# Optimization experiments

Measured on AMD Instinct MI355X. Metric: run time of the kernel, lower is better.

## Reference

```python
import jax, jax.numpy as jnp
import numpy as np

CHUNK = 64  # chunk_size from init


def _fused_chunk_fwd(q, k, v, scale, chunk):
    # q,k,v: [B,S,H,D]
    B, S, H, D = q.shape
    NT = S // chunk
    # -> [NT, B, H, chunk, D] for scan over chunks
    def to_chunks(x):
        return x.reshape(B, NT, chunk, H, D).transpose(1, 0, 3, 2, 4)
    qc, kc, vc = to_chunks(q), to_chunks(k), to_chunks(v)
    mask = jnp.tril(jnp.ones((chunk, chunk), dtype=q.dtype))  # row >= col (inclusive)

    def step(h, xs):
        qi, ki, vi = xs  # each [B,H,chunk,D]
        qs = qi * scale
        # intra-chunk causal attention scores (no softmax: linear attention)
        s = jnp.einsum('bhqd,bhkd->bhqk', qs, ki) * mask
        # intra-chunk contribution + inter-chunk recurrent state contribution
        o = jnp.einsum('bhqk,bhke->bhqe', s, vi) + jnp.einsum('bhqd,bhde->bhqe', qs, h)
        # state update: h += K^T V  (strictly after producing this chunk's output)
        h = h + jnp.einsum('bhcd,bhce->bhde', ki, vi)
        return h, o

    h0 = jnp.zeros((B, H, D, D), dtype=jnp.float32)
    hf, oc = jax.lax.scan(step, h0, (qc, kc, vc))
    # oc: [NT,B,H,chunk,D] -> [B,S,H,D]
    o = oc.transpose(1, 0, 3, 2, 4).reshape(B, S, H, D)
    return o, hf


def setup_inputs() -> dict:
    key = jax.random.key(0)
    kq, kk, kv = jax.random.split(key, 3)
    B, S, H, D = 2, 4096, 16, 128
    q = jax.random.normal(kq, (B, S, H, D), dtype=jnp.float32)
    k = jax.random.normal(kk, (B, S, H, D), dtype=jnp.float32)
    v = jax.random.normal(kv, (B, S, H, D), dtype=jnp.float32)
    return {"q": q, "k": k, "v": v}


def reference(q, k, v):
    D = q.shape[-1]
    scale = D ** (-0.5)
    o, final_state = _fused_chunk_fwd(q, k, v, scale, CHUNK)
    return o, final_state
```

## Files before the change

### kernel.cpp

```cpp
#include <hip/hip_runtime.h>
#include <math.h>

#define BB 2
#define SS 4096
#define HH 16
#define DD 128
#define CK 64
#define NTC 64
#define HD 2048
#define SQ 136
#define ST 72

typedef __attribute__((ext_vector_type(8))) short bh8;
typedef __attribute__((ext_vector_type(16))) float fx16;

#define MFMA32(a, b, c) __builtin_amdgcn_mfma_f32_32x32x16_bf16(a, b, c, 0, 0, 0)

__device__ inline unsigned short f2bf(float f) {
    unsigned int u = __float_as_uint(f);
    return (unsigned short)((u + 0x7FFFu + ((u >> 16) & 1u)) >> 16);
}
__device__ inline unsigned int pk2(float a, float b) {
    return (unsigned int)f2bf(a) | ((unsigned int)f2bf(b) << 16);
}

#define SWAP32(x, y) asm("v_permlane32_swap_b32 %0, %1" : "+v"(x), "+v"(y))

#define MKFRAG(dst, cc, O) { \
    unsigned a0_ = pk2(cc[(O)+0], cc[(O)+1]), a1_ = pk2(cc[(O)+2], cc[(O)+3]); \
    unsigned a2_ = pk2(cc[(O)+4], cc[(O)+5]), a3_ = pk2(cc[(O)+6], cc[(O)+7]); \
    SWAP32(a0_, a2_); SWAP32(a1_, a3_); \
    union { unsigned u[4]; bh8 v; } r_; \
    r_.u[0] = a0_; r_.u[1] = a1_; r_.u[2] = a2_; r_.u[3] = a3_; \
    dst = r_.v; }

__global__ __launch_bounds__(512, 4) void ksum_kernel(const float* __restrict__ k,
                                                      const float* __restrict__ v,
                                                      float* __restrict__ G,
                                                      int CPG, int NG) {
    int g = blockIdx.x, h = blockIdx.y, b = blockIdx.z;
    int t = threadIdx.x, l = t & 63, w = t >> 6, hi = l >> 5, lm = l & 31;
    int dbp = 2 * (w >> 2), eb = w & 3;
    __shared__ short lkT[2][128 * ST];
    __shared__ short lvT[2][128 * ST];
    fx16 h0 = {}, h1 = {};
    long hbase = ((long)b * SS) * HD + (long)h * DD;
    float kt[16], vt[16];

#define KLOAD(cc) { long base_ = hbase + (long)(g * CPG + (cc)) * CK * HD; \
    _Pragma("unroll") for (int i = 0; i < 8; ++i) { int it = t + 512 * i; \
        int e = (it & 31) + 32 * (it >> 10); int c2 = (it >> 5) & 31; \
        long ga = base_ + (long)(2 * c2) * HD + e; \
        kt[2*i] = k[ga]; kt[2*i+1] = k[ga + HD]; \
        vt[2*i] = v[ga]; vt[2*i+1] = v[ga + HD]; } }

#define KSTAGE(pn) { \
    _Pragma("unroll") for (int i = 0; i < 8; ++i) { int it = t + 512 * i; \
        int e = (it & 31) + 32 * (it >> 10); int c2 = (it >> 5) & 31; \
        *(unsigned*)&lkT[pn][e * ST + 2 * c2] = pk2(kt[2*i], kt[2*i+1]); \
        *(unsigned*)&lvT[pn][e * ST + 2 * c2] = pk2(vt[2*i], vt[2*i+1]); } }

    KLOAD(0); KSTAGE(0); if (CPG > 1) KLOAD(1);
    __syncthreads();
    int p = 0;
    for (int c = 0; c < CPG; ++c) {
        if (c + 1 < CPG) KSTAGE(p ^ 1);
        if (c + 2 < CPG) KLOAD(c + 2);
        bh8 Bv0 = *(const bh8*)&lvT[p][(32*eb+lm)*ST +  0 + 8*hi];
        bh8 Bv1 = *(const bh8*)&lvT[p][(32*eb+lm)*ST + 16 + 8*hi];
        bh8 Bv2 = *(const bh8*)&lvT[p][(32*eb+lm)*ST + 32 + 8*hi];
        bh8 Bv3 = *(const bh8*)&lvT[p][(32*eb+lm)*ST + 48 + 8*hi];
#define KM4(hx, db) { \
        bh8 A0_ = *(const bh8*)&lkT[p][(32*(db)+lm)*ST +  0 + 8*hi]; hx = MFMA32(A0_, Bv0, hx); \
        bh8 A1_ = *(const bh8*)&lkT[p][(32*(db)+lm)*ST + 16 + 8*hi]; hx = MFMA32(A1_, Bv1, hx); \
        bh8 A2_ = *(const bh8*)&lkT[p][(32*(db)+lm)*ST + 32 + 8*hi]; hx = MFMA32(A2_, Bv2, hx); \
        bh8 A3_ = *(const bh8*)&lkT[p][(32*(db)+lm)*ST + 48 + 8*hi]; hx = MFMA32(A3_, Bv3, hx); }
        KM4(h0, dbp) KM4(h1, dbp + 1)
        __syncthreads();
        p ^= 1;
    }
    float* Gp = G + ((long)(b * HH + h) * NG + g) * (DD * DD);
    long t0 = (long)((dbp) * 4 + eb) * 1024 + l * 16;
    long t1 = (long)((dbp + 1) * 4 + eb) * 1024 + l * 16;
#pragma unroll
    for (int q4 = 0; q4 < 4; ++q4) {
        *(float4*)&Gp[t0 + 4*q4] = make_float4(h0[4*q4], h0[4*q4+1], h0[4*q4+2], h0[4*q4+3]);
        *(float4*)&Gp[t1 + 4*q4] = make_float4(h1[4*q4], h1[4*q4+1], h1[4*q4+2], h1[4*q4+3]);
    }
}

__global__ __launch_bounds__(256) void prefix_kernel(float* __restrict__ G,
                                                     float* __restrict__ hf,
                                                     int NG) {
    int tid = blockIdx.x * 256 + threadIdx.x;
    int bh = tid >> 11;
    int fl = (tid & 2047) * 8;
    float* Gb = G + (long)bh * NG * (DD * DD) + fl;
    float4 a0 = make_float4(0.f, 0.f, 0.f, 0.f), a1 = a0;
    for (int g = 0; g < NG; ++g) {
        float* p = Gb + (long)g * (DD * DD);
        float4 v0 = *(float4*)p;
        float4 v1 = *(float4*)(p + 4);
        *(float4*)p       = a0;
        *(float4*)(p + 4) = a1;
        a0.x += v0.x; a0.y += v0.y; a0.z += v0.z; a0.w += v0.w;
        a1.x += v1.x; a1.y += v1.y; a1.z += v1.z; a1.w += v1.w;
    }
    float acc[8] = {a0.x, a0.y, a0.z, a0.w, a1.x, a1.y, a1.z, a1.w};
    float* hb = hf + (long)bh * (DD * DD);
    int tile = fl >> 10, li = (fl >> 4) & 63;
#pragma unroll
    for (int j = 0; j < 8; ++j) {
        int rg = (fl & 15) + j;
        int d = 32 * (tile >> 2) + (rg & 3) + 8 * (rg >> 2) + 4 * (li >> 5);
        int e = 32 * (tile & 3) + (li & 31);
        hb[d * DD + e] = acc[j];
    }
}

__global__ __launch_bounds__(512, 2) void scan_kernel(const float* __restrict__ q,
                                                      const float* __restrict__ kk,
                                                      const float* __restrict__ vv,
                                                      const float* __restrict__ G,
                                                      float* __restrict__ o,
                                                      int CPG, int NG, float scale) {
    int g = blockIdx.x, h = blockIdx.y, b = blockIdx.z;
    int t = threadIdx.x, l = t & 63, w = t >> 6, hi = l >> 5, lm = l & 31;
    int rb = w >> 2, eb = w & 3;
    __shared__ short lq [2][64 * SQ];
    __shared__ short lk [2][64 * SQ];
    __shared__ short lkT[2][128 * ST];
    __shared__ short lvT[2][128 * ST];

    fx16 h0 = {}, h1 = {}, h2 = {}, h3 = {};
    {
        const float* Gp = G + ((long)(b * HH + h) * NG + g) * (DD * DD);
#define GINIT(hx, db) { const float* p_ = Gp + (long)((db) * 4 + eb) * 1024 + l * 16; \
        _Pragma("unroll") for (int q4 = 0; q4 < 4; ++q4) { \
            float4 x_ = *(const float4*)&p_[4*q4]; \
            hx[4*q4] = x_.x; hx[4*q4+1] = x_.y; hx[4*q4+2] = x_.z; hx[4*q4+3] = x_.w; } }
        GINIT(h0, 0) GINIT(h1, 1) GINIT(h2, 2) GINIT(h3, 3)
    }

    long hbase = ((long)b * SS) * HD + (long)h * DD;
    float4 qv[4], kv[4];
    float kt[16], vt[16];
    int r8 = t >> 3, c8 = t & 7;

#define SLOAD(cc) { long base_ = hbase + (long)(g * CPG + (cc)) * CK * HD; \
    _Pragma("unroll") for (int j = 0; j < 4; ++j) { \
        long ga = base_ + (long)r8 * HD + 4 * c8 + 32 * j; \
        qv[j] = *(const float4*)&q[ga]; kv[j] = *(const float4*)&kk[ga]; } \
    _Pragma("unroll") for (int i = 0; i < 8; ++i) { int it = t + 512 * i; \
        int e = (it & 31) + 32 * (it >> 10); int c2 = (it >> 5) & 31; \
        long ga = base_ + (long)(2 * c2) * HD + e; \
        kt[2*i] = kk[ga]; kt[2*i+1] = kk[ga + HD]; \
        vt[2*i] = vv[ga]; vt[2*i+1] = vv[ga + HD]; } }

#define SSTAGE(pn) { \
    _Pragma("unroll") for (int j = 0; j < 4; ++j) { \
        uint2 uq_; uq_.x = pk2(qv[j].x * scale, qv[j].y * scale); \
        uq_.y = pk2(qv[j].z * scale, qv[j].w * scale); \
        *(uint2*)&lq[pn][r8 * SQ + 4 * c8 + 32 * j] = uq_; \
        uint2 uk_; uk_.x = pk2(kv[j].x, kv[j].y); uk_.y = pk2(kv[j].z, kv[j].w); \
        *(uint2*)&lk[pn][r8 * SQ + 4 * c8 + 32 * j] = uk_; } \
    _Pragma("unroll") for (int i = 0; i < 8; ++i) { int it = t + 512 * i; \
        int e = (it & 31) + 32 * (it >> 10); int c2 = (it >> 5) & 31; \
        *(unsigned*)&lkT[pn][e * ST + 2 * c2] = pk2(kt[2*i], kt[2*i+1]); \
        *(unsigned*)&lvT[pn][e * ST + 2 * c2] = pk2(vt[2*i], vt[2*i+1]); } }

    SLOAD(0); SSTAGE(0); if (CPG > 1) SLOAD(1);
    __syncthreads();
    int p = 0;

    for (int c = 0; c < CPG; ++c) {
        long base = hbase + (long)(g * CPG + c) * CK * HD;
        if (c + 1 < CPG) SSTAGE(p ^ 1);

        fx16 sa0 = {}, sa1 = {};
#pragma unroll
        for (int ks = 0; ks < 8; ++ks) {
            bh8 Bq = *(const bh8*)&lq[p][(32*rb+lm)*SQ + 16*ks + 8*hi];
            bh8 A0 = *(const bh8*)&lk[p][lm*SQ + 16*ks + 8*hi];
            sa0 = MFMA32(A0, Bq, sa0);
            if (rb) {
                bh8 A1 = *(const bh8*)&lk[p][(32+lm)*SQ + 16*ks + 8*hi];
                sa1 = MFMA32(A1, Bq, sa1);
            }
        }
        bh8 fS0, fS1, fS2, fS3;
        {
            float ms[16];
            int rr = 32 * rb + lm;
            if (rb == 0) {
#pragma unroll
                for (int rg = 0; rg < 16; ++rg) {
                    int cc_ = (rg & 3) + 8 * (rg >> 2) + 4 * hi;
                    ms[rg] = (cc_ <= rr) ? sa0[rg] : 0.f;
                }
                MKFRAG(fS0, ms, 0) MKFRAG(fS1, ms, 8)
                fS2 = fS0; fS3 = fS1;
            } else {
                MKFRAG(fS0, sa0, 0) MKFRAG(fS1, sa0, 8)
#pragma unroll
                for (int rg = 0; rg < 16; ++rg) {
                    int cc_ = 32 + (rg & 3) + 8 * (rg >> 2) + 4 * hi;
                    ms[rg] = (cc_ <= rr) ? sa1[rg] : 0.f;
                }
                MKFRAG(fS2, ms, 0) MKFRAG(fS3, ms, 8)
            }
        }
        if (c + 2 < CPG) SLOAD(c + 2);

        bh8 Bv0 = *(const bh8*)&lvT[p][(32*eb+lm)*ST +  0 + 8*hi];
        bh8 Bv1 = *(const bh8*)&lvT[p][(32*eb+lm)*ST + 16 + 8*hi];
        bh8 Bv2 = *(const bh8*)&lvT[p][(32*eb+lm)*ST + 32 + 8*hi];
        bh8 Bv3 = *(const bh8*)&lvT[p][(32*eb+lm)*ST + 48 + 8*hi];

        fx16 oa = {};
        oa = MFMA32(fS0, Bv0, oa);
        oa = MFMA32(fS1, Bv1, oa);
        if (rb) {
            oa = MFMA32(fS2, Bv2, oa);
            oa = MFMA32(fS3, Bv3, oa);
        }
#define M3STEP(hx, db) { \
        bh8 Aq0 = *(const bh8*)&lq[p][(32*rb+lm)*SQ + 16*(2*(db)) + 8*hi]; \
        bh8 Bh0; MKFRAG(Bh0, hx, 0); oa = MFMA32(Aq0, Bh0, oa); \
        bh8 Aq1 = *(const bh8*)&lq[p][(32*rb+lm)*SQ + 16*(2*(db)+1) + 8*hi]; \
        bh8 Bh1; MKFRAG(Bh1, hx, 8); oa = MFMA32(Aq1, Bh1, oa); }
        M3STEP(h0, 0) M3STEP(h1, 1) M3STEP(h2, 2) M3STEP(h3, 3)

#define M4STEP(hx, db) { \
        bh8 A0_ = *(const bh8*)&lkT[p][(32*(db)+lm)*ST +  0 + 8*hi]; hx = MFMA32(A0_, Bv0, hx); \
        bh8 A1_ = *(const bh8*)&lkT[p][(32*(db)+lm)*ST + 16 + 8*hi]; hx = MFMA32(A1_, Bv1, hx); \
        bh8 A2_ = *(const bh8*)&lkT[p][(32*(db)+lm)*ST + 32 + 8*hi]; hx = MFMA32(A2_, Bv2, hx); \
        bh8 A3_ = *(const bh8*)&lkT[p][(32*(db)+lm)*ST + 48 + 8*hi]; hx = MFMA32(A3_, Bv3, hx); }
        M4STEP(h0, 0) M4STEP(h1, 1) M4STEP(h2, 2) M4STEP(h3, 3)

        {
            float* op = o + base;
            int e = 32 * eb + lm;
#pragma unroll
            for (int rg = 0; rg < 16; ++rg) {
                int r = 32 * rb + (rg & 3) + 8 * (rg >> 2) + 4 * hi;
                op[(long)r * HD + e] = oa[rg];
            }
        }
        __syncthreads();
        p ^= 1;
    }
}

extern "C" void kernel_launch(void* const* d_in, const int* in_sizes, int n_in,
                              void* d_out, int out_size, void* d_ws, size_t ws_size,
                              hipStream_t stream) {
    const float* q = (const float*)d_in[0];
    const float* k = (const float*)d_in[1];
    const float* v = (const float*)d_in[2];
    float* o  = (float*)d_out;
    float* hf = o + (long)BB * SS * HH * DD;
    float* G  = (float*)d_ws;

    int NG = 8;
    while (NG > 1 && (size_t)BB * HH * NG * DD * DD * 4 > ws_size) NG >>= 1;
    int CPG = NTC / NG;
    float scale = 1.0f / sqrtf((float)DD);

    ksum_kernel<<<dim3(NG, HH, BB), 512, 0, stream>>>(k, v, G, CPG, NG);
    prefix_kernel<<<dim3(256, 1, 1), 256, 0, stream>>>(G, hf, NG);
    scan_kernel<<<dim3(NG, HH, BB), 512, 0, stream>>>(q, k, v, G, o, CPG, NG, scale);
}
```

Measured before the change: 97.07 us.

## Store chunk-group states in bf16, swizzle LDS, single-buffer scan, raise groups

```diff
diff --git a/kernel.cpp b/kernel.cpp
--- a/kernel.cpp
+++ b/kernel.cpp
@@ -1,4 +1,5 @@
 #include <hip/hip_runtime.h>
+#include <hip/hip_bf16.h>
 #include <math.h>
 
 #define BB 2
@@ -15,14 +16,15 @@
 typedef __attribute__((ext_vector_type(16))) float fx16;
 
 #define MFMA32(a, b, c) __builtin_amdgcn_mfma_f32_32x32x16_bf16(a, b, c, 0, 0, 0)
-
-__device__ inline unsigned short f2bf(float f) {
-    unsigned int u = __float_as_uint(f);
-    return (unsigned short)((u + 0x7FFFu + ((u >> 16) & 1u)) >> 16);
-}
-__device__ inline unsigned int pk2(float a, float b) {
-    return (unsigned int)f2bf(a) | ((unsigned int)f2bf(b) << 16);
-}
+#define SWZ(off, row) ((off) ^ (8 * (((row) >> 3) & 3)))
+
+__device__ inline unsigned pk2(float a, float b) {
+    union { __hip_bfloat162 h2; unsigned u; } r;
+    r.h2.x = __float2bfloat16(a);
+    r.h2.y = __float2bfloat16(b);
+    return r.u;
+}
+#define UPK(u, x, y) { x = __uint_as_float((unsigned)(u) << 16); y = __uint_as_float((unsigned)(u) & 0xFFFF0000u); }
 
 #define SWAP32(x, y) asm("v_permlane32_swap_b32 %0, %1" : "+v"(x), "+v"(y))
 
@@ -36,7 +38,7 @@
 
 __global__ __launch_bounds__(512, 4) void ksum_kernel(const float* __restrict__ k,
                                                       const float* __restrict__ v,
-                                                      float* __restrict__ G,
+                                                      unsigned* __restrict__ G,
                                                       int CPG, int NG) {
     int g = blockIdx.x, h = blockIdx.y, b = blockIdx.z;
     int t = threadIdx.x, l = t & 63, w = t >> 6, hi = l >> 5, lm = l & 31;
@@ -57,8 +59,8 @@
 #define KSTAGE(pn) { \
     _Pragma("unroll") for (int i = 0; i < 8; ++i) { int it = t + 512 * i; \
         int e = (it & 31) + 32 * (it >> 10); int c2 = (it >> 5) & 31; \
-        *(unsigned*)&lkT[pn][e * ST + 2 * c2] = pk2(kt[2*i], kt[2*i+1]); \
-        *(unsigned*)&lvT[pn][e * ST + 2 * c2] = pk2(vt[2*i], vt[2*i+1]); } }
+        *(unsigned*)&lkT[pn][e * ST + SWZ(2 * c2, e)] = pk2(kt[2*i], kt[2*i+1]); \
+        *(unsigned*)&lvT[pn][e * ST + SWZ(2 * c2, e)] = pk2(vt[2*i], vt[2*i+1]); } }
 
     KLOAD(0); KSTAGE(0); if (CPG > 1) KLOAD(1);
     __syncthreads();
@@ -66,47 +68,57 @@
     for (int c = 0; c < CPG; ++c) {
         if (c + 1 < CPG) KSTAGE(p ^ 1);
         if (c + 2 < CPG) KLOAD(c + 2);
-        bh8 Bv0 = *(const bh8*)&lvT[p][(32*eb+lm)*ST +  0 + 8*hi];
-        bh8 Bv1 = *(const bh8*)&lvT[p][(32*eb+lm)*ST + 16 + 8*hi];
-        bh8 Bv2 = *(const bh8*)&lvT[p][(32*eb+lm)*ST + 32 + 8*hi];
-        bh8 Bv3 = *(const bh8*)&lvT[p][(32*eb+lm)*ST + 48 + 8*hi];
+        bh8 Bv0 = *(const bh8*)&lvT[p][(32*eb+lm)*ST + SWZ( 0 + 8*hi, lm)];
+        bh8 Bv1 = *(const bh8*)&lvT[p][(32*eb+lm)*ST + SWZ(16 + 8*hi, lm)];
+        bh8 Bv2 = *(const bh8*)&lvT[p][(32*eb+lm)*ST + SWZ(32 + 8*hi, lm)];
+        bh8 Bv3 = *(const bh8*)&lvT[p][(32*eb+lm)*ST + SWZ(48 + 8*hi, lm)];
+        __builtin_amdgcn_s_setprio(1);
 #define KM4(hx, db) { \
-        bh8 A0_ = *(const bh8*)&lkT[p][(32*(db)+lm)*ST +  0 + 8*hi]; hx = MFMA32(A0_, Bv0, hx); \
-        bh8 A1_ = *(const bh8*)&lkT[p][(32*(db)+lm)*ST + 16 + 8*hi]; hx = MFMA32(A1_, Bv1, hx); \
-        bh8 A2_ = *(const bh8*)&lkT[p][(32*(db)+lm)*ST + 32 + 8*hi]; hx = MFMA32(A2_, Bv2, hx); \
-        bh8 A3_ = *(const bh8*)&lkT[p][(32*(db)+lm)*ST + 48 + 8*hi]; hx = MFMA32(A3_, Bv3, hx); }
+        bh8 A0_ = *(const bh8*)&lkT[p][(32*(db)+lm)*ST + SWZ( 0 + 8*hi, lm)]; hx = MFMA32(A0_, Bv0, hx); \
+        bh8 A1_ = *(const bh8*)&lkT[p][(32*(db)+lm)*ST + SWZ(16 + 8*hi, lm)]; hx = MFMA32(A1_, Bv1, hx); \
+        bh8 A2_ = *(const bh8*)&lkT[p][(32*(db)+lm)*ST + SWZ(32 + 8*hi, lm)]; hx = MFMA32(A2_, Bv2, hx); \
+        bh8 A3_ = *(const bh8*)&lkT[p][(32*(db)+lm)*ST + SWZ(48 + 8*hi, lm)]; hx = MFMA32(A3_, Bv3, hx); }
         KM4(h0, dbp) KM4(h1, dbp + 1)
+        __builtin_amdgcn_s_setprio(0);
         __syncthreads();
         p ^= 1;
     }
-    float* Gp = G + ((long)(b * HH + h) * NG + g) * (DD * DD);
-    long t0 = (long)((dbp) * 4 + eb) * 1024 + l * 16;
-    long t1 = (long)((dbp + 1) * 4 + eb) * 1024 + l * 16;
-#pragma unroll
-    for (int q4 = 0; q4 < 4; ++q4) {
-        *(float4*)&Gp[t0 + 4*q4] = make_float4(h0[4*q4], h0[4*q4+1], h0[4*q4+2], h0[4*q4+3]);
-        *(float4*)&Gp[t1 + 4*q4] = make_float4(h1[4*q4], h1[4*q4+1], h1[4*q4+2], h1[4*q4+3]);
-    }
-}
-
-__global__ __launch_bounds__(256) void prefix_kernel(float* __restrict__ G,
+    unsigned* Gp = G + ((long)(b * HH + h) * NG + g) * (DD * DD / 2);
+    long t0 = (long)(dbp * 4 + eb) * 512 + l * 8;
+    long t1 = (long)((dbp + 1) * 4 + eb) * 512 + l * 8;
+    uint4 u;
+    u.x = pk2(h0[0],h0[1]);  u.y = pk2(h0[2],h0[3]);  u.z = pk2(h0[4],h0[5]);  u.w = pk2(h0[6],h0[7]);
+    *(uint4*)(Gp + t0) = u;
+    u.x = pk2(h0[8],h0[9]);  u.y = pk2(h0[10],h0[11]); u.z = pk2(h0[12],h0[13]); u.w = pk2(h0[14],h0[15]);
+    *(uint4*)(Gp + t0 + 4) = u;
+    u.x = pk2(h1[0],h1[1]);  u.y = pk2(h1[2],h1[3]);  u.z = pk2(h1[4],h1[5]);  u.w = pk2(h1[6],h1[7]);
+    *(uint4*)(Gp + t1) = u;
+    u.x = pk2(h1[8],h1[9]);  u.y = pk2(h1[10],h1[11]); u.z = pk2(h1[12],h1[13]); u.w = pk2(h1[14],h1[15]);
+    *(uint4*)(Gp + t1 + 4) = u;
+}
+
+__global__ __launch_bounds__(256) void prefix_kernel(unsigned* __restrict__ G,
                                                      float* __restrict__ hf,
                                                      int NG) {
     int tid = blockIdx.x * 256 + threadIdx.x;
     int bh = tid >> 11;
     int fl = (tid & 2047) * 8;
-    float* Gb = G + (long)bh * NG * (DD * DD) + fl;
-    float4 a0 = make_float4(0.f, 0.f, 0.f, 0.f), a1 = a0;
+    unsigned* Gb = G + (long)bh * NG * (DD * DD / 2) + fl / 2;
+    float a[8] = {0.f, 0.f, 0.f, 0.f, 0.f, 0.f, 0.f, 0.f};
+    uint4 nxt = *(uint4*)Gb;
     for (int g = 0; g < NG; ++g) {
-        float* p = Gb + (long)g * (DD * DD);
-        float4 v0 = *(float4*)p;
-        float4 v1 = *(float4*)(p + 4);
-        *(float4*)p       = a0;
-        *(float4*)(p + 4) = a1;
-        a0.x += v0.x; a0.y += v0.y; a0.z += v0.z; a0.w += v0.w;
-        a1.x += v1.x; a1.y += v1.y; a1.z += v1.z; a1.w += v1.w;
-    }
-    float acc[8] = {a0.x, a0.y, a0.z, a0.w, a1.x, a1.y, a1.z, a1.w};
+        uint4 cur = nxt;
+        if (g + 1 < NG) nxt = *(uint4*)(Gb + (long)(g + 1) * (DD * DD / 2));
+        uint4 st;
+        st.x = pk2(a[0], a[1]); st.y = pk2(a[2], a[3]);
+        st.z = pk2(a[4], a[5]); st.w = pk2(a[6], a[7]);
+        *(uint4*)(Gb + (long)g * (DD * DD / 2)) = st;
+        float x, y;
+        UPK(cur.x, x, y); a[0] += x; a[1] += y;
+        UPK(cur.y, x, y); a[2] += x; a[3] += y;
+        UPK(cur.z, x, y); a[4] += x; a[5] += y;
+        UPK(cur.w, x, y); a[6] += x; a[7] += y;
+    }
     float* hb = hf + (long)bh * (DD * DD);
     int tile = fl >> 10, li = (fl >> 4) & 63;
 #pragma unroll
@@ -114,108 +126,101 @@
         int rg = (fl & 15) + j;
         int d = 32 * (tile >> 2) + (rg & 3) + 8 * (rg >> 2) + 4 * (li >> 5);
         int e = 32 * (tile & 3) + (li & 31);
-        hb[d * DD + e] = acc[j];
-    }
-}
-
-__global__ __launch_bounds__(512, 2) void scan_kernel(const float* __restrict__ q,
+        hb[d * DD + e] = a[j];
+    }
+}
+
+__global__ __launch_bounds__(512, 4) void scan_kernel(const float* __restrict__ q,
                                                       const float* __restrict__ kk,
                                                       const float* __restrict__ vv,
-                                                      const float* __restrict__ G,
+                                                      const unsigned* __restrict__ G,
                                                       float* __restrict__ o,
                                                       int CPG, int NG, float scale) {
     int g = blockIdx.x, h = blockIdx.y, b = blockIdx.z;
     int t = threadIdx.x, l = t & 63, w = t >> 6, hi = l >> 5, lm = l & 31;
     int rb = w >> 2, eb = w & 3;
-    __shared__ short lq [2][64 * SQ];
-    __shared__ short lk [2][64 * SQ];
-    __shared__ short lkT[2][128 * ST];
-    __shared__ short lvT[2][128 * ST];
+    __shared__ short lq [64 * SQ];
+    __shared__ short lk [64 * SQ];
+    __shared__ short lkT[128 * ST];
+    __shared__ short lvT[128 * ST];
 
     fx16 h0 = {}, h1 = {}, h2 = {}, h3 = {};
     {
-        const float* Gp = G + ((long)(b * HH + h) * NG + g) * (DD * DD);
-#define GINIT(hx, db) { const float* p_ = Gp + (long)((db) * 4 + eb) * 1024 + l * 16; \
-        _Pragma("unroll") for (int q4 = 0; q4 < 4; ++q4) { \
-            float4 x_ = *(const float4*)&p_[4*q4]; \
-            hx[4*q4] = x_.x; hx[4*q4+1] = x_.y; hx[4*q4+2] = x_.z; hx[4*q4+3] = x_.w; } }
+        const unsigned* Gp = G + ((long)(b * HH + h) * NG + g) * (DD * DD / 2);
+#define GINIT(hx, db) { const unsigned* p_ = Gp + (long)((db) * 4 + eb) * 512 + l * 8; \
+        uint4 u0 = *(const uint4*)p_; uint4 u1 = *(const uint4*)(p_ + 4); \
+        UPK(u0.x, hx[0], hx[1]);  UPK(u0.y, hx[2], hx[3]); \
+        UPK(u0.z, hx[4], hx[5]);  UPK(u0.w, hx[6], hx[7]); \
+        UPK(u1.x, hx[8], hx[9]);  UPK(u1.y, hx[10], hx[11]); \
+        UPK(u1.z, hx[12], hx[13]); UPK(u1.w, hx[14], hx[15]); }
         GINIT(h0, 0) GINIT(h1, 1) GINIT(h2, 2) GINIT(h3, 3)
     }
 
     long hbase = ((long)b * SS) * HD + (long)h * DD;
-    float4 qv[4], kv[4];
-    float kt[16], vt[16];
     int r8 = t >> 3, c8 = t & 7;
-
-#define SLOAD(cc) { long base_ = hbase + (long)(g * CPG + (cc)) * CK * HD; \
-    _Pragma("unroll") for (int j = 0; j < 4; ++j) { \
-        long ga = base_ + (long)r8 * HD + 4 * c8 + 32 * j; \
-        qv[j] = *(const float4*)&q[ga]; kv[j] = *(const float4*)&kk[ga]; } \
-    _Pragma("unroll") for (int i = 0; i < 8; ++i) { int it = t + 512 * i; \
-        int e = (it & 31) + 32 * (it >> 10); int c2 = (it >> 5) & 31; \
-        long ga = base_ + (long)(2 * c2) * HD + e; \
-        kt[2*i] = kk[ga]; kt[2*i+1] = kk[ga + HD]; \
-        vt[2*i] = vv[ga]; vt[2*i+1] = vv[ga + HD]; } }
-
-#define SSTAGE(pn) { \
-    _Pragma("unroll") for (int j = 0; j < 4; ++j) { \
-        uint2 uq_; uq_.x = pk2(qv[j].x * scale, qv[j].y * scale); \
-        uq_.y = pk2(qv[j].z * scale, qv[j].w * scale); \
-        *(uint2*)&lq[pn][r8 * SQ + 4 * c8 + 32 * j] = uq_; \
-        uint2 uk_; uk_.x = pk2(kv[j].x, kv[j].y); uk_.y = pk2(kv[j].z, kv[j].w); \
-        *(uint2*)&lk[pn][r8 * SQ + 4 * c8 + 32 * j] = uk_; } \
-    _Pragma("unroll") for (int i = 0; i < 8; ++i) { int it = t + 512 * i; \
-        int e = (it & 31) + 32 * (it >> 10); int c2 = (it >> 5) & 31; \
-        *(unsigned*)&lkT[pn][e * ST + 2 * c2] = pk2(kt[2*i], kt[2*i+1]); \
-        *(unsigned*)&lvT[pn][e * ST + 2 * c2] = pk2(vt[2*i], vt[2*i+1]); } }
-
-    SLOAD(0); SSTAGE(0); if (CPG > 1) SLOAD(1);
-    __syncthreads();
-    int p = 0;
 
     for (int c = 0; c < CPG; ++c) {
         long base = hbase + (long)(g * CPG + c) * CK * HD;
-        if (c + 1 < CPG) SSTAGE(p ^ 1);
-
-        fx16 sa0 = {}, sa1 = {};
+#pragma unroll
+        for (int j = 0; j < 4; ++j) {
+            long ga = base + (long)r8 * HD + 4 * c8 + 32 * j;
+            float4 qv = *(const float4*)&q[ga];
+            float4 kv = *(const float4*)&kk[ga];
+            uint2 uq; uq.x = pk2(qv.x * scale, qv.y * scale); uq.y = pk2(qv.z * scale, qv.w * scale);
+            *(uint2*)&lq[r8 * SQ + SWZ(4 * c8 + 32 * j, r8)] = uq;
+            uint2 uk; uk.x = pk2(kv.x, kv.y); uk.y = pk2(kv.z, kv.w);
+            *(uint2*)&lk[r8 * SQ + SWZ(4 * c8 + 32 * j, r8)] = uk;
+        }
+#pragma unroll
+        for (int i = 0; i < 8; ++i) {
+            int it = t + 512 * i;
+            int e = (it & 31) + 32 * (it >> 10);
+            int c2 = (it >> 5) & 31;
+            long ga = base + (long)(2 * c2) * HD + e;
+            *(unsigned*)&lkT[e * ST + SWZ(2 * c2, e)] = pk2(kk[ga], kk[ga + HD]);
+            *(unsigned*)&lvT[e * ST + SWZ(2 * c2, e)] = pk2(vv[ga], vv[ga + HD]);
+        }
+        __syncthreads();
+
+        __builtin_amdgcn_s_setprio(1);
+        fx16 sa = {};
 #pragma unroll
         for (int ks = 0; ks < 8; ++ks) {
-            bh8 Bq = *(const bh8*)&lq[p][(32*rb+lm)*SQ + 16*ks + 8*hi];
-            bh8 A0 = *(const bh8*)&lk[p][lm*SQ + 16*ks + 8*hi];
-            sa0 = MFMA32(A0, Bq, sa0);
-            if (rb) {
-                bh8 A1 = *(const bh8*)&lk[p][(32+lm)*SQ + 16*ks + 8*hi];
-                sa1 = MFMA32(A1, Bq, sa1);
-            }
+            bh8 Bq = *(const bh8*)&lq[(32*rb+lm)*SQ + SWZ(16*ks + 8*hi, lm)];
+            bh8 A0 = *(const bh8*)&lk[lm*SQ + SWZ(16*ks + 8*hi, lm)];
+            sa = MFMA32(A0, Bq, sa);
         }
         bh8 fS0, fS1, fS2, fS3;
-        {
+        if (rb == 0) {
             float ms[16];
-            int rr = 32 * rb + lm;
-            if (rb == 0) {
-#pragma unroll
-                for (int rg = 0; rg < 16; ++rg) {
-                    int cc_ = (rg & 3) + 8 * (rg >> 2) + 4 * hi;
-                    ms[rg] = (cc_ <= rr) ? sa0[rg] : 0.f;
-                }
-                MKFRAG(fS0, ms, 0) MKFRAG(fS1, ms, 8)
-                fS2 = fS0; fS3 = fS1;
-            } else {
-                MKFRAG(fS0, sa0, 0) MKFRAG(fS1, sa0, 8)
-#pragma unroll
-                for (int rg = 0; rg < 16; ++rg) {
-                    int cc_ = 32 + (rg & 3) + 8 * (rg >> 2) + 4 * hi;
-                    ms[rg] = (cc_ <= rr) ? sa1[rg] : 0.f;
-                }
-                MKFRAG(fS2, ms, 0) MKFRAG(fS3, ms, 8)
-            }
-        }
-        if (c + 2 < CPG) SLOAD(c + 2);
-
-        bh8 Bv0 = *(const bh8*)&lvT[p][(32*eb+lm)*ST +  0 + 8*hi];
-        bh8 Bv1 = *(const bh8*)&lvT[p][(32*eb+lm)*ST + 16 + 8*hi];
-        bh8 Bv2 = *(const bh8*)&lvT[p][(32*eb+lm)*ST + 32 + 8*hi];
-        bh8 Bv3 = *(const bh8*)&lvT[p][(32*eb+lm)*ST + 48 + 8*hi];
+#pragma unroll
+            for (int rg = 0; rg < 16; ++rg) {
+                int cc_ = (rg & 3) + 8 * (rg >> 2) + 4 * hi;
+                ms[rg] = (cc_ <= lm) ? sa[rg] : 0.f;
+            }
+            MKFRAG(fS0, ms, 0) MKFRAG(fS1, ms, 8)
+        } else {
+            MKFRAG(fS0, sa, 0) MKFRAG(fS1, sa, 8)
+            fx16 sb = {};
+#pragma unroll
+            for (int ks = 0; ks < 8; ++ks) {
+                bh8 Bq = *(const bh8*)&lq[(32+lm)*SQ + SWZ(16*ks + 8*hi, lm)];
+                bh8 A1 = *(const bh8*)&lk[(32+lm)*SQ + SWZ(16*ks + 8*hi, lm)];
+                sb = MFMA32(A1, Bq, sb);
+            }
+            float ms[16];
+#pragma unroll
+            for (int rg = 0; rg < 16; ++rg) {
+                int cc_ = 32 + (rg & 3) + 8 * (rg >> 2) + 4 * hi;
+                ms[rg] = (cc_ <= 32 + lm) ? sb[rg] : 0.f;
+            }
+            MKFRAG(fS2, ms, 0) MKFRAG(fS3, ms, 8)
+        }
+
+        bh8 Bv0 = *(const bh8*)&lvT[(32*eb+lm)*ST + SWZ( 0 + 8*hi, lm)];
+        bh8 Bv1 = *(const bh8*)&lvT[(32*eb+lm)*ST + SWZ(16 + 8*hi, lm)];
+        bh8 Bv2 = *(const bh8*)&lvT[(32*eb+lm)*ST + SWZ(32 + 8*hi, lm)];
+        bh8 Bv3 = *(const bh8*)&lvT[(32*eb+lm)*ST + SWZ(48 + 8*hi, lm)];
 
         fx16 oa = {};
         oa = MFMA32(fS0, Bv0, oa);
@@ -225,18 +230,19 @@
             oa = MFMA32(fS3, Bv3, oa);
         }
 #define M3STEP(hx, db) { \
-        bh8 Aq0 = *(const bh8*)&lq[p][(32*rb+lm)*SQ + 16*(2*(db)) + 8*hi]; \
+        bh8 Aq0 = *(const bh8*)&lq[(32*rb+lm)*SQ + SWZ(16*(2*(db)) + 8*hi, lm)]; \
         bh8 Bh0; MKFRAG(Bh0, hx, 0); oa = MFMA32(Aq0, Bh0, oa); \
-        bh8 Aq1 = *(const bh8*)&lq[p][(32*rb+lm)*SQ + 16*(2*(db)+1) + 8*hi]; \
+        bh8 Aq1 = *(const bh8*)&lq[(32*rb+lm)*SQ + SWZ(16*(2*(db)+1) + 8*hi, lm)]; \
         bh8 Bh1; MKFRAG(Bh1, hx, 8); oa = MFMA32(Aq1, Bh1, oa); }
         M3STEP(h0, 0) M3STEP(h1, 1) M3STEP(h2, 2) M3STEP(h3, 3)
 
 #define M4STEP(hx, db) { \
-        bh8 A0_ = *(const bh8*)&lkT[p][(32*(db)+lm)*ST +  0 + 8*hi]; hx = MFMA32(A0_, Bv0, hx); \
-        bh8 A1_ = *(const bh8*)&lkT[p][(32*(db)+lm)*ST + 16 + 8*hi]; hx = MFMA32(A1_, Bv1, hx); \
-        bh8 A2_ = *(const bh8*)&lkT[p][(32*(db)+lm)*ST + 32 + 8*hi]; hx = MFMA32(A2_, Bv2, hx); \
-        bh8 A3_ = *(const bh8*)&lkT[p][(32*(db)+lm)*ST + 48 + 8*hi]; hx = MFMA32(A3_, Bv3, hx); }
+        bh8 A0_ = *(const bh8*)&lkT[(32*(db)+lm)*ST + SWZ( 0 + 8*hi, lm)]; hx = MFMA32(A0_, Bv0, hx); \
+        bh8 A1_ = *(const bh8*)&lkT[(32*(db)+lm)*ST + SWZ(16 + 8*hi, lm)]; hx = MFMA32(A1_, Bv1, hx); \
+        bh8 A2_ = *(const bh8*)&lkT[(32*(db)+lm)*ST + SWZ(32 + 8*hi, lm)]; hx = MFMA32(A2_, Bv2, hx); \
+        bh8 A3_ = *(const bh8*)&lkT[(32*(db)+lm)*ST + SWZ(48 + 8*hi, lm)]; hx = MFMA32(A3_, Bv3, hx); }
         M4STEP(h0, 0) M4STEP(h1, 1) M4STEP(h2, 2) M4STEP(h3, 3)
+        __builtin_amdgcn_s_setprio(0);
 
         {
             float* op = o + base;
@@ -248,7 +254,6 @@
             }
         }
         __syncthreads();
-        p ^= 1;
     }
 }
 
@@ -260,10 +265,10 @@
     const float* v = (const float*)d_in[2];
     float* o  = (float*)d_out;
     float* hf = o + (long)BB * SS * HH * DD;
-    float* G  = (float*)d_ws;
-
-    int NG = 8;
-    while (NG > 1 && (size_t)BB * HH * NG * DD * DD * 4 > ws_size) NG >>= 1;
+    unsigned* G = (unsigned*)d_ws;
+
+    int NG = 16;
+    while (NG > 1 && (size_t)BB * HH * NG * DD * DD * 2 > ws_size) NG >>= 1;
     int CPG = NTC / NG;
     float scale = 1.0f / sqrtf((float)DD);
 
```

New measurement: 360.0 us. 271% more time.
